# Optimization experiments

Measured on AMD Instinct MI355X. Metric: run time of the kernel, lower is better.

The kernel has to match this reference:

```python
import jax, jax.numpy as jnp
import numpy as np

NUM_V = 20000
N_EDGES = 160000
IN_CH, OUT_CH = 16, 32
IN_ORDER = OUT_ORDER = MID_ORDER = 2
N_RINGS = 2
BAND_LIMIT = 2
NUM_SAMPLES = 7


def build_kernel_basis(n_in, n_out, bl):
    """Equivariant kernel basis [num_bases, 2*bl+1, 2*n_out+1, 2*n_in+1].
    Freq axis layout: [const, cos(t), sin(t), cos(2t), sin(2t), ...] matching precomp."""
    Din, Dout, F = 2 * n_in + 1, 2 * n_out + 1, 2 * bl + 1
    I = np.eye(2)
    E = np.array([[0., -1.], [1., 0.]])   # rotation by pi/2
    S = np.array([[1., 0.], [0., -1.]])   # reflection
    ES = E @ S
    sl = lambda m: slice(0, 1) if m == 0 else slice(2 * m - 1, 2 * m + 1)
    bases = []

    def add(f, cos_blk, sin_blk, m, n):
        if f > bl:
            return
        B = np.zeros((F, Dout, Din))
        if f == 0:
            B[0, sl(m), sl(n)] = cos_blk
        else:
            B[2 * f - 1, sl(m), sl(n)] = cos_blk
            B[2 * f, sl(m), sl(n)] = sin_blk
        bases.append(B)

    for m in range(n_out + 1):
        for n in range(n_in + 1):
            if m == 0 and n == 0:
                add(0, np.ones((1, 1)), None, 0, 0)
            elif n == 0:  # scalar -> order-m pair: R(m t) e1, R(m t) e2
                add(m, np.array([[1.], [0.]]), np.array([[0.], [1.]]), m, 0)
                add(m, np.array([[0.], [1.]]), np.array([[-1.], [0.]]), m, 0)
            elif m == 0:  # order-n pair -> scalar: rows of R(-n t)
                add(n, np.array([[1., 0.]]), np.array([[0., 1.]]), 0, n)
                add(n, np.array([[0., 1.]]), np.array([[-1., 0.]]), 0, n)
            else:
                d = m - n
                f = abs(d)
                sg = 1.0 if d >= 0 else -1.0
                add(f, I, sg * E, m, n)          # R(d t)
                add(f, E, -sg * I, m, n)         # R(d t + pi/2)
                add(m + n, S, ES, m, n)          # R((m+n) t) S
                add(m + n, ES, -S, m, n)         # R((m+n) t + pi/2) S
    return np.stack(bases).astype(np.float32)


def fourier_mats(order, n):
    th = 2 * np.pi * np.arange(n) / n
    cols = [np.ones(n)]
    for m in range(1, order + 1):
        cols += [np.cos(m * th), np.sin(m * th)]
    T = np.stack(cols, 1)                              # [n_samples, 2*order+1]
    scale = np.array([1.0] + [2.0] * (2 * order)) / n
    Tinv = (T * scale).T                               # [2*order+1, n_samples]
    return jnp.asarray(T, jnp.float32), jnp.asarray(Tinv, jnp.float32)


def rep_act(x, alpha, order):
    """Gauge transport: rotate order-m feature pairs by m*alpha. x: [E,C,2*order+1]."""
    parts = [x[:, :, :1]]
    for m in range(1, order + 1):
        c = jnp.cos(m * alpha)[:, None]
        s = jnp.sin(m * alpha)[:, None]
        a, b = x[:, :, 2 * m - 1], x[:, :, 2 * m]
        parts.append(jnp.stack([c * a - s * b, s * a + c * b], axis=-1))
    return jnp.concatenate(parts, axis=-1)


def gem_conv(x, edge_index, precomp, connection, K, W, b, in_order):
    src, dst = edge_index[1], edge_index[0]
    xt = rep_act(x[src], connection, in_order)               # [E, Cin, Din] gather + transport
    wk = jnp.einsum('bfij,broc->froicj', K, W)               # fold basis with ring weights (small)
    t = jnp.einsum('ecj,froicj->efroi', xt, wk)              # per-edge freq/ring responses
    msg = jnp.einsum('efr,efroi->eoi', precomp, t)           # [E, Cout, Dout]
    out = jax.ops.segment_sum(msg, dst, num_segments=NUM_V)  # scatter-add to vertices
    return out.at[:, :, 0].add(b)                            # bias on scalar component


def regular_relu(x, order):
    T, Tinv = fourier_mats(order, NUM_SAMPLES)
    s = jnp.einsum('vcd,sd->vcs', x, T)   # irrep -> regular samples
    return jnp.einsum('vcs,ds->vcd', jax.nn.relu(s), Tinv)


def setup_inputs() -> dict:
    key = jax.random.key(0)
    k = jax.random.split(key, 8)
    nb = build_kernel_basis(IN_ORDER, MID_ORDER, BAND_LIMIT).shape[0]  # 19
    Din = 2 * IN_ORDER + 1
    x = jax.random.normal(k[0], (NUM_V, IN_CH, Din), jnp.float32)
    edge_index = jax.random.randint(k[1], (2, N_EDGES), 0, NUM_V, dtype=jnp.int32)
    precomp = jax.random.normal(k[2], (N_EDGES, 2 * BAND_LIMIT + 1, N_RINGS), jnp.float32)
    connection = jax.random.uniform(k[3], (N_EDGES,), jnp.float32) * (2 * np.pi)
    W1 = jax.random.normal(k[4], (nb, N_RINGS, OUT_CH, IN_CH), jnp.float32) * 0.1
    W2 = jax.random.normal(k[5], (nb, N_RINGS, OUT_CH, OUT_CH), jnp.float32) * 0.05
    W_lin = jax.random.normal(k[6], (OUT_CH, IN_CH), jnp.float32) * 0.1
    zeros = lambda: jnp.zeros((OUT_CH,), jnp.float32)
    return {"x": x, "edge_index": edge_index, "precomp": precomp, "connection": connection,
            "W1": W1, "b1": zeros(), "W2": W2, "b2": zeros(), "W_lin": W_lin, "b_lin": zeros()}


def reference(x, edge_index, precomp, connection, W1, b1, W2, b2, W_lin, b_lin):
    K = jnp.asarray(build_kernel_basis(IN_ORDER, MID_ORDER, BAND_LIMIT))  # orders equal -> shared basis
    y = gem_conv(x, edge_index, precomp, connection, K, W1, b1, IN_ORDER)
    y = regular_relu(y, MID_ORDER)
    y = gem_conv(y, edge_index, precomp, connection, K, W2, b2, MID_ORDER)
    res = jnp.einsum('vcd,oc->vod', x, W_lin) + b_lin[None, :, None]  # 1x1 conv residual
    o = min(y.shape[2], res.shape[2])
    y = y.at[:, :, :o].add(res[:, :, :o])
    return regular_relu(y, OUT_ORDER)
```

## Files before the change

kernel.cpp:

```cpp
#include <hip/hip_runtime.h>
#include <hip/hip_bf16.h>
#include <cstdint>

#define NV     20000
#define NE     160000
#define IC1    16
#define OC     32
#define DIN    5
#define NSLOT  49
#define NOUT   160
#define YSTR   165
struct SlotTables {
    int n;
    int b[64], f[64], i[64], j[64];
    float v[64];
};

constexpr SlotTables make_slots() {
    SlotTables T{};
    float K[19][5][5][5] = {};
    int nb = 0;
    const int BL = 2;
    auto add = [&](int f, const float (*cb)[2], const float (*sb)[2],
                   int m, int n) {
        if (f > BL) return;
        int r0 = (m == 0) ? 0 : (2 * m - 1), nr = (m == 0) ? 1 : 2;
        int c0 = (n == 0) ? 0 : (2 * n - 1), nc = (n == 0) ? 1 : 2;
        for (int a = 0; a < nr; a++)
            for (int bb = 0; bb < nc; bb++) {
                if (f == 0) {
                    K[nb][0][r0 + a][c0 + bb] = cb[a][bb];
                } else {
                    K[nb][2 * f - 1][r0 + a][c0 + bb] = cb[a][bb];
                    K[nb][2 * f    ][r0 + a][c0 + bb] = sb[a][bb];
                }
            }
        nb++;
    };
    const float ONE[2][2]  = {{1, 0}, {0, 0}};
    const float I2[2][2]   = {{1, 0}, {0, 1}};
    const float E2[2][2]   = {{0, -1}, {1, 0}};
    const float S2[2][2]   = {{1, 0}, {0, -1}};
    const float ES2[2][2]  = {{0, 1}, {1, 0}};
    const float NS2[2][2]  = {{-1, 0}, {0, 1}};
    const float C10[2][2]  = {{1, 0}, {0, 0}};
    const float C01[2][2]  = {{0, 0}, {1, 0}};
    const float CM10[2][2] = {{-1, 0}, {0, 0}};
    const float R10[2][2]  = {{1, 0}, {0, 0}};
    const float R01[2][2]  = {{0, 1}, {0, 0}};
    const float RM10[2][2] = {{-1, 0}, {0, 0}};

    for (int m = 0; m <= 2; m++)
        for (int n = 0; n <= 2; n++) {
            if (m == 0 && n == 0) {
                add(0, ONE, ONE, 0, 0);
            } else if (n == 0) {
                add(m, C10, C01, m, 0);
                add(m, C01, CM10, m, 0);
            } else if (m == 0) {
                add(n, R10, R01, 0, n);
                add(n, R01, RM10, 0, n);
            } else {
                int d = m - n;
                int f = d >= 0 ? d : -d;
                float sg = d >= 0 ? 1.f : -1.f;
                const float sgE[2][2]  = {{0, -sg}, {sg, 0}};
                const float msgI[2][2] = {{-sg, 0}, {0, -sg}};
                add(f, I2, sgE, m, n);
                add(f, E2, msgI, m, n);
                add(m + n, S2, ES2, m, n);
                add(m + n, ES2, NS2, m, n);
            }
        }
    T.n = 0;
    for (int i = 0; i < 5; i++)
        for (int b = 0; b < nb; b++)
            for (int f = 0; f < 5; f++)
                for (int j = 0; j < 5; j++)
                    if (K[b][f][i][j] != 0.0f) {
                        T.b[T.n] = b; T.f[T.n] = f; T.i[T.n] = i;
                        T.j[T.n] = j; T.v[T.n] = K[b][f][i][j];
                        T.n++;
                    }
    return T;
}

constexpr SlotTables SL = make_slots();
static_assert(SL.n == NSLOT, "expect 49 kernel-basis nonzeros");

__device__ __forceinline__ uint32_t bf16_rne(float f) {
    uint32_t u = __float_as_uint(f);
    u += 0x7fffu + ((u >> 16) & 1u);
    return u >> 16;
}

typedef __attribute__((ext_vector_type(8))) short bf16x8;
typedef __attribute__((ext_vector_type(4))) float f32x4;

template<int C>
__global__ __launch_bounds__(256) void build_M(const float* __restrict__ W,
                                               float* __restrict__ M) {
    int t = blockIdx.x * 256 + threadIdx.x;
    const int K = C * 50;
    if (t >= K * NOUT) return;
    int n = t % NOUT, k = t / NOUT;
    int o = n / 5, i = n % 5;
    int c = k / 50, r50 = k % 50;
    int j = r50 / 10, q = r50 % 10;
    int f = q >> 1, r = q & 1;
    float acc = 0.f;
    #pragma unroll
    for (int s = 0; s < NSLOT; s++) {
        if (SL.j[s] == j && SL.f[s] == f && SL.i[s] == i)
            acc += SL.v[s] * W[(size_t)((SL.b[s] * 2 + r) * 32 + o) * C + c];
    }
    M[(size_t)k * NOUT + n] = acc;
}

template<int K>
__global__ __launch_bounds__(256) void build_Mfrag(const float* __restrict__ M,
                                                   uint32_t* __restrict__ Mf) {
    int t = blockIdx.x * 256 + threadIdx.x;
    const int total = (K / 32) * 10 * 64 * 4;
    if (t >= total) return;
    int a = t & 3;
    int idx = t >> 2;
    int lane = idx & 63; idx >>= 6;
    int nt = idx % 10;
    int ck = idx / 10;
    int col = nt * 16 + (lane & 15);
    int k0 = ck * 32 + (lane >> 4) * 8 + 2 * a;
    uint32_t lo = bf16_rne(M[(size_t)k0 * NOUT + col]);
    uint32_t hi = bf16_rne(M[(size_t)(k0 + 1) * NOUT + col]);
    Mf[t] = lo | (hi << 16);
}

__global__ __launch_bounds__(256) void hist_k(const int* __restrict__ ei,
                                              int* __restrict__ counts) {
    int e = blockIdx.x * 256 + threadIdx.x;
    if (e < NE) atomicAdd(&counts[ei[e]], 1);
}

__global__ __launch_bounds__(1024) void scan_k(const int* __restrict__ counts,
                                               int* __restrict__ cursor) {
    __shared__ int part[1024];
    int t = threadIdx.x;
    int base = t * 20;
    int local[20];
    int s = 0;
    #pragma unroll
    for (int k = 0; k < 20; k++) {
        int idx = base + k;
        int c = (idx < NV) ? counts[idx] : 0;
        local[k] = c; s += c;
    }
    part[t] = s;
    __syncthreads();
    for (int off = 1; off < 1024; off <<= 1) {
        int add = (t >= off) ? part[t - off] : 0;
        __syncthreads();
        part[t] += add;
        __syncthreads();
    }
    int run = (t == 0) ? 0 : part[t - 1];
    #pragma unroll
    for (int k = 0; k < 20; k++) {
        int idx = base + k;
        if (idx < NV) { cursor[idx] = run; run += local[k]; }
    }
}

__global__ __launch_bounds__(256) void scatter_pack(const int* __restrict__ ei,
                                                    const float* __restrict__ pre,
                                                    const float* __restrict__ conn,
                                                    int* __restrict__ cursor,
                                                    int* __restrict__ SRC,
                                                    float4* __restrict__ REC) {
    int e = blockIdx.x * 256 + threadIdx.x;
    if (e == 0) {
        SRC[NE] = 0;
        REC[(size_t)NE * 3 + 0] = float4{0.f, 0.f, 0.f, 0.f};
        REC[(size_t)NE * 3 + 1] = float4{0.f, 0.f, 0.f, 0.f};
        REC[(size_t)NE * 3 + 2] = float4{0.f, 0.f, 0.f, 0.f};
    }
    if (e >= NE) return;
    int pos = atomicAdd(&cursor[ei[e]], 1);
    SRC[pos] = ei[NE + e];
    float al = conn[e];
    float c1 = __cosf(al), s1 = __sinf(al);
    const float* pp = pre + (size_t)e * 10;
    REC[(size_t)pos * 3 + 0] = float4{c1, s1, pp[0], pp[1]};
    REC[(size_t)pos * 3 + 1] = float4{pp[2], pp[3], pp[4], pp[5]};
    REC[(size_t)pos * 3 + 2] = float4{pp[6], pp[7], pp[8], pp[9]};
}

__global__ __launch_bounds__(256) void x_pack(const float* __restrict__ x,
                                              uint4* __restrict__ xb) {
    int t = blockIdx.x * 256 + threadIdx.x;
    if (t >= NV * IC1) return;
    const float* xr = x + (size_t)t * 5;
    uint4 o;
    o.x = bf16_rne(xr[0]) | (bf16_rne(xr[1]) << 16);
    o.y = bf16_rne(xr[2]) | (bf16_rne(xr[3]) << 16);
    o.z = bf16_rne(xr[4]);
    o.w = 0;
    xb[t] = o;
}

template<int C>
__global__ __launch_bounds__(256) void zbuild6(const uint4* __restrict__ xb,
                                               const int*   __restrict__ SRC,
                                               const float4* __restrict__ REC,
                                               const int* __restrict__ cursor,
                                               uint32_t* __restrict__ Z,
                                               int v0, int v1) {
    __shared__ uint32_t st[3200];
    int tid = threadIdx.x;
    int t = blockIdx.x * 256 + tid;
    int pair = t >> 1, h = t & 1;
    int npairs = (v1 - v0) * C;
    bool valid = pair < npairs;
    int c = pair % C;
    int v = v0 + (valid ? pair / C : 0);
    int beg = 0, end = 0;
    if (valid) { beg = (v == 0) ? 0 : cursor[v - 1]; end = cursor[v]; }

    float acc[25];
    #pragma unroll
    for (int z = 0; z < 25; z++) acc[z] = 0.f;

    int k = beg;
    if (k < end) {
        int k1 = (k + 1 < end) ? k + 1 : NE;
        int k2 = (k + 2 < end) ? k + 2 : NE;
        int s0 = SRC[k], s1i = SRC[k1], s2i = SRC[k2];
        const float4* rp = REC + (size_t)k * 3;
        float4 r0 = rp[0], r1 = rp[1], r2 = rp[2];
        uint4 u0 = xb[(size_t)s0 * C + c];
        uint4 u1 = xb[(size_t)s1i * C + c];
        while (true) {
            bool more = (k1 != NE);
            int k3 = (k + 3 < end) ? k + 3 : NE;
            int s3i = SRC[k3];
            uint4 u2 = xb[(size_t)s2i * C + c];
            const float4* rpn = REC + (size_t)k1 * 3;
            float4 n0 = rpn[0], n1 = rpn[1], n2 = rpn[2];
            float x0 = __uint_as_float(u0.x << 16);
            float x1 = __uint_as_float(u0.x & 0xffff0000u);
            float x2 = __uint_as_float(u0.y << 16);
            float x3 = __uint_as_float(u0.y & 0xffff0000u);
            float x4 = __uint_as_float(u0.z << 16);
            float cc1 = r0.x, ss1 = r0.y;
            float cc2 = cc1 * cc1 - ss1 * ss1, ss2 = 2.f * cc1 * ss1;
            float xt[5];
            xt[0] = x0;
            xt[1] = cc1 * x1 - ss1 * x2;
            xt[2] = ss1 * x1 + cc1 * x2;
            xt[3] = cc2 * x3 - ss2 * x4;
            xt[4] = ss2 * x3 + cc2 * x4;
            float ph[5];
            ph[0] = h ? r1.w : r0.z;
            ph[1] = h ? r2.x : r0.w;
            ph[2] = h ? r2.y : r1.x;
            ph[3] = h ? r2.z : r1.y;
            ph[4] = h ? r2.w : r1.z;
            #pragma unroll
            for (int j = 0; j < 5; j++)
                #pragma unroll
                for (int w = 0; w < 5; w++)
                    acc[j * 5 + w] = fmaf(xt[j], ph[w], acc[j * 5 + w]);
            if (!more) break;
            k = k1; k1 = k2; k2 = k3;
            r0 = n0; r1 = n1; r2 = n2;
            u0 = u1; u1 = u2;
            s2i = s3i;
        }
    }
    uint32_t* sb = st + (tid >> 1) * 25;
    #pragma unroll
    for (int j = 0; j < 5; j++) {
        float q5v = __shfl_xor(acc[j * 5 + 0], 1);
        if (h == 0) {
            sb[j * 5 + 0] = bf16_rne(acc[j * 5 + 0]) | (bf16_rne(acc[j * 5 + 1]) << 16);
            sb[j * 5 + 1] = bf16_rne(acc[j * 5 + 2]) | (bf16_rne(acc[j * 5 + 3]) << 16);
            sb[j * 5 + 2] = bf16_rne(acc[j * 5 + 4]) | (bf16_rne(q5v) << 16);
        } else {
            sb[j * 5 + 3] = bf16_rne(acc[j * 5 + 1]) | (bf16_rne(acc[j * 5 + 2]) << 16);
            sb[j * 5 + 4] = bf16_rne(acc[j * 5 + 3]) | (bf16_rne(acc[j * 5 + 4]) << 16);
        }
    }
    __syncthreads();
    size_t gbase = (size_t)blockIdx.x * 3200;
    int pbase = blockIdx.x * 128;
    for (int i = tid; i < 3200; i += 256)
        if (pbase + i / 25 < npairs) Z[gbase + i] = st[i];
}

__device__ __forceinline__ void fourier_relu(float d0, float d1, float d2,
                                             float d3, float d4, float* out5) {
    float o0 = 0, o1 = 0, o2 = 0, o3 = 0, o4 = 0;
    #pragma unroll
    for (int k = 0; k < 7; k++) {
        float th = (float)k * (6.28318530717958647692f / 7.0f);
        float ck = __cosf(th), sk = __sinf(th);
        float c2k = ck * ck - sk * sk, s2k = 2.f * ck * sk;
        float sv = d0 + ck * d1 + sk * d2 + c2k * d3 + s2k * d4;
        sv = fmaxf(sv, 0.f);
        o0 += sv; o1 += sv * ck; o2 += sv * sk; o3 += sv * c2k; o4 += sv * s2k;
    }
    const float i7 = 1.0f / 7.0f;
    out5[0] = o0 * i7; out5[1] = o1 * (2.f * i7); out5[2] = o2 * (2.f * i7);
    out5[3] = o3 * (2.f * i7); out5[4] = o4 * (2.f * i7);
}

template<int K, int EPI>
__global__ __launch_bounds__(256) void gemm_fused(const uint32_t* __restrict__ Z,
                                                  const uint32_t* __restrict__ Mf,
                                                  int rows,
                                                  uint4* __restrict__ y1b,
                                                  const float* __restrict__ bias,
                                                  const float* __restrict__ xres,
                                                  const float* __restrict__ Wl,
                                                  const float* __restrict__ bl,
                                                  float* __restrict__ outp) {
    constexpr int NC = K / 32;
    constexpr int NCH0 = (NC + 1) / 2;
    __shared__ float Ys[16 * YSTR];
    __shared__ float Xs[EPI == 2 ? 16 * 80 : 1];
    int t = threadIdx.x;
    int lane = t & 63;
    int wave = t >> 6;
    int nh = wave & 1, kh = wave >> 1;
    int r0 = blockIdx.x * 16;
    int mrow = lane & 15;
    int q = lane >> 4;
    int ra = r0 + mrow;
    if (ra >= rows) ra = rows - 1;
    const uint32_t* za = Z + (size_t)ra * (K / 2) + q * 4;
    const bf16x8* mfg = (const bf16x8*)((const uint4*)Mf + lane);

    int cka = kh ? NCH0 : 0;
    int ckz = kh ? NC : NCH0;
    int ntb = nh * 5;

    f32x4 acc[5];
    #pragma unroll
    for (int nt = 0; nt < 5; nt++) acc[nt] = {0.f, 0.f, 0.f, 0.f};

    bf16x8 af = *(const bf16x8*)(za + (size_t)cka * 16);
    bf16x8 bfr[5];
    #pragma unroll
    for (int nt = 0; nt < 5; nt++)
        bfr[nt] = mfg[((size_t)cka * 10 + ntb + nt) * 64];

    for (int ck = cka; ck < ckz; ck++) {
        bf16x8 afn = af;
        bf16x8 bfn[5];
        #pragma unroll
        for (int nt = 0; nt < 5; nt++) bfn[nt] = bfr[nt];
        if (ck + 1 < ckz) {
            afn = *(const bf16x8*)(za + (size_t)(ck + 1) * 16);
            #pragma unroll
            for (int nt = 0; nt < 5; nt++)
                bfn[nt] = mfg[((size_t)(ck + 1) * 10 + ntb + nt) * 64];
        }
        #pragma unroll
        for (int nt = 0; nt < 5; nt++)
            acc[nt] = __builtin_amdgcn_mfma_f32_16x16x32_bf16(af, bfr[nt],
                                                              acc[nt], 0, 0, 0);
        af = afn;
        #pragma unroll
        for (int nt = 0; nt < 5; nt++) bfr[nt] = bfn[nt];
    }

    if (EPI == 2) {
        int gbase = blockIdx.x * 16 * 80;
        int glim = rows * 80;
        for (int i = t; i < 16 * 80; i += 256)
            Xs[i] = (gbase + i < glim) ? xres[gbase + i] : 0.f;
    }
    if (kh == 0) {
        #pragma unroll
        for (int nt = 0; nt < 5; nt++) {
            int col = (ntb + nt) * 16 + mrow;
            #pragma unroll
            for (int reg = 0; reg < 4; reg++)
                Ys[(q * 4 + reg) * YSTR + col] = acc[nt][reg];
        }
    }
    __syncthreads();
    if (kh == 1) {
        #pragma unroll
        for (int nt = 0; nt < 5; nt++) {
            int col = (ntb + nt) * 16 + mrow;
            #pragma unroll
            for (int reg = 0; reg < 4; reg++)
                Ys[(q * 4 + reg) * YSTR + col] += acc[nt][reg];
        }
    }
    __syncthreads();
    #pragma unroll
    for (int it = 0; it < 2; it++) {
        int item = t + it * 256;
        int row = item >> 5, ch = item & 31;
        int vr = blockIdx.x * 16 + row;
        if (vr >= rows) continue;
        const float* yr = &Ys[row * YSTR + ch * 5];
        float d0 = yr[0], d1 = yr[1], d2 = yr[2], d3 = yr[3], d4 = yr[4];
        float r5[5];
        if (EPI == 1) {
            d0 += bias[ch];
            fourier_relu(d0, d1, d2, d3, d4, r5);
            uint4 o;
            o.x = bf16_rne(r5[0]) | (bf16_rne(r5[1]) << 16);
            o.y = bf16_rne(r5[2]) | (bf16_rne(r5[3]) << 16);
            o.z = bf16_rne(r5[4]);
            o.w = 0;
            y1b[(size_t)vr * 32 + ch] = o;
        } else {
            float rr0 = 0, rr1 = 0, rr2 = 0, rr3 = 0, rr4 = 0;
            const float* xs = &Xs[row * 80];
            const float* wl = Wl + ch * IC1;
            #pragma unroll
            for (int c = 0; c < IC1; c++) {
                float w = wl[c];
                rr0 = fmaf(w, xs[c * 5 + 0], rr0);
                rr1 = fmaf(w, xs[c * 5 + 1], rr1);
                rr2 = fmaf(w, xs[c * 5 + 2], rr2);
                rr3 = fmaf(w, xs[c * 5 + 3], rr3);
                rr4 = fmaf(w, xs[c * 5 + 4], rr4);
            }
            float blo = bl[ch];
            d0 += bias[ch] + rr0 + blo;
            d1 += rr1 + blo;
            d2 += rr2 + blo;
            d3 += rr3 + blo;
            d4 += rr4 + blo;
            fourier_relu(d0, d1, d2, d3, d4, r5);
            float* ob = outp + ((size_t)vr * 32 + ch) * 5;
            #pragma unroll
            for (int d = 0; d < 5; d++) ob[d] = r5[d];
        }
    }
}

extern "C" void kernel_launch(void* const* d_in, const int* in_sizes, int n_in,
                              void* d_out, int out_size, void* d_ws, size_t ws_size,
                              hipStream_t stream) {
    const float* x    = (const float*)d_in[0];
    const int*   ei   = (const int*)  d_in[1];
    const float* pre  = (const float*)d_in[2];
    const float* conn = (const float*)d_in[3];
    const float* W1   = (const float*)d_in[4];
    const float* b1   = (const float*)d_in[5];
    const float* W2   = (const float*)d_in[6];
    const float* b2   = (const float*)d_in[7];
    const float* Wl   = (const float*)d_in[8];
    const float* bl   = (const float*)d_in[9];
    float* out = (float*)d_out;

    const int K1 = IC1 * 50;
    const int K2 = OC  * 50;

    const size_t Y_BYTES   = (size_t)NV * NOUT * sizeof(float);
    const size_t M1_BYTES  = (size_t)K1 * NOUT * sizeof(float);
    const size_t M2_BYTES  = (size_t)K2 * NOUT * sizeof(float);
    const size_t MF1_BYTES = (size_t)(K1 / 32) * 10 * 64 * 16;
    const size_t MF2_BYTES = (size_t)(K2 / 32) * 10 * 64 * 16;
    const size_t CSR_BYTES = (size_t)(2 * NV) * sizeof(int);
    const size_t REC_BYTES = (size_t)(NE + 1) * 48;
    const size_t SRC_BYTES = (((size_t)(NE + 1) * 4 + 15) / 16) * 16;
    const size_t Y1B_BYTES = (size_t)NV * OC * 16;
    char* ws = (char*)d_ws;
    float* M1 = (float*)(ws);
    float* M2 = (float*)(ws + M1_BYTES);
    uint32_t* Mf1 = (uint32_t*)(ws + M1_BYTES + M2_BYTES);
    uint32_t* Mf2 = (uint32_t*)(ws + M1_BYTES + M2_BYTES + MF1_BYTES);
    int* counts = (int*)(ws + M1_BYTES + M2_BYTES + MF1_BYTES + MF2_BYTES);
    int* cursor = counts + NV;
    size_t csr_end = M1_BYTES + M2_BYTES + MF1_BYTES + MF2_BYTES + CSR_BYTES;
    float4* REC = (float4*)(ws + csr_end);
    int*    SRC = (int*)(ws + csr_end + REC_BYTES);
    uint4*  Y1B = (uint4*)(ws + csr_end + REC_BYTES + SRC_BYTES);
    uint4*  XB1 = Y1B;
    size_t fixed = csr_end + REC_BYTES + SRC_BYTES + Y1B_BYTES;

    size_t tail = (ws_size > fixed) ? (ws_size - fixed) : 0;
    uint32_t* zbuf;
    size_t zcap;
    if (tail >= Y_BYTES) { zbuf = (uint32_t*)(ws + fixed); zcap = tail; }
    else                 { zbuf = (uint32_t*)d_out;        zcap = Y_BYTES; }
    int chunk1 = (int)(zcap / ((size_t)K1 * 2)); if (chunk1 > NV) chunk1 = NV;
    int chunk2 = (int)(zcap / ((size_t)K2 * 2)); if (chunk2 > NV) chunk2 = NV;
    int nch1 = (NV + chunk1 - 1) / chunk1; chunk1 = (NV + nch1 - 1) / nch1;
    int nch2 = (NV + chunk2 - 1) / chunk2; chunk2 = (NV + nch2 - 1) / nch2;

    hipMemsetAsync(counts, 0, NV * sizeof(int), stream);

    build_M<IC1><<<(K1 * NOUT + 255) / 256, 256, 0, stream>>>(W1, M1);
    build_M<OC> <<<(K2 * NOUT + 255) / 256, 256, 0, stream>>>(W2, M2);
    build_Mfrag<K1><<<((K1 / 32) * 2560 + 255) / 256, 256, 0, stream>>>(M1, Mf1);
    build_Mfrag<K2><<<((K2 / 32) * 2560 + 255) / 256, 256, 0, stream>>>(M2, Mf2);

    hist_k<<<(NE + 255) / 256, 256, 0, stream>>>(ei, counts);
    scan_k<<<1, 1024, 0, stream>>>(counts, cursor);
    scatter_pack<<<(NE + 255) / 256, 256, 0, stream>>>(ei, pre, conn, cursor,
                                                       SRC, REC);
    x_pack<<<(NV * IC1 + 255) / 256, 256, 0, stream>>>(x, XB1);

    for (int v0 = 0; v0 < NV; v0 += chunk1) {
        int v1 = v0 + chunk1; if (v1 > NV) v1 = NV;
        int rows = v1 - v0;
        zbuild6<IC1><<<((size_t)rows * IC1 * 2 + 255) / 256, 256, 0, stream>>>(
            XB1, SRC, REC, cursor, zbuf, v0, v1);
        gemm_fused<K1, 1><<<(rows + 15) / 16, 256, 0, stream>>>(
            zbuf, Mf1, rows, Y1B + (size_t)v0 * 32, b1,
            nullptr, nullptr, nullptr, nullptr);
    }
    for (int v0 = 0; v0 < NV; v0 += chunk2) {
        int v1 = v0 + chunk2; if (v1 > NV) v1 = NV;
        int rows = v1 - v0;
        zbuild6<OC><<<((size_t)rows * OC * 2 + 255) / 256, 256, 0, stream>>>(
            Y1B, SRC, REC, cursor, zbuf, v0, v1);
        gemm_fused<K2, 2><<<(rows + 15) / 16, 256, 0, stream>>>(
            zbuf, Mf2, rows, nullptr, b2,
            x + (size_t)v0 * (IC1 * DIN), Wl, bl, out + (size_t)v0 * NOUT);
    }
}
```

Measured before the change: 257.4 us.

## Split GEMM K-loop across four wave groups and stage A rows in LDS

The fused GEMM kernel now runs 512 threads, splitting the K reduction four ways instead of two so each block has more waves in flight. The A-operand rows for the block are first loaded cooperatively into shared memory with coalesced 16-byte loads, and the MFMA loop then reads them from LDS. Partial sums from the four K groups are combined serially into the shared Y tile, which adds barriers. The epilogue maps one thread per (row, channel) item. Costs are more shared memory per block, extra synchronization, and possibly lower occupancy.

Result: faster. 248.2 us (-3.6%).

```diff
diff --git a/kernel.cpp b/kernel.cpp
--- a/kernel.cpp
+++ b/kernel.cpp
@@ -314,7 +314,7 @@
 }
 
 template<int K, int EPI>
-__global__ __launch_bounds__(256) void gemm_fused(const uint32_t* __restrict__ Z,
+__global__ __launch_bounds__(512) void gemm_fused(const uint32_t* __restrict__ Z,
                                                   const uint32_t* __restrict__ Mf,
                                                   int rows,
                                                   uint4* __restrict__ y1b,
@@ -324,7 +324,9 @@
                                                   const float* __restrict__ bl,
                                                   float* __restrict__ outp) {
     constexpr int NC = K / 32;
-    constexpr int NCH0 = (NC + 1) / 2;
+    constexpr int ZROW = K / 8;
+    constexpr int ZPAD = K / 2 + 4;
+    __shared__ uint32_t Za[16 * ZPAD];
     __shared__ float Ys[16 * YSTR];
     __shared__ float Xs[EPI == 2 ? 16 * 80 : 1];
     int t = threadIdx.x;
@@ -334,41 +336,47 @@
     int r0 = blockIdx.x * 16;
     int mrow = lane & 15;
     int q = lane >> 4;
-    int ra = r0 + mrow;
-    if (ra >= rows) ra = rows - 1;
-    const uint32_t* za = Z + (size_t)ra * (K / 2) + q * 4;
+
+    {
+        int total = 16 * ZROW;
+        for (int g = t; g < total; g += 512) {
+            int row = g / ZROW, off = g % ZROW;
+            int gr = r0 + row; if (gr >= rows) gr = rows - 1;
+            uint4 v = ((const uint4*)Z)[(size_t)gr * ZROW + off];
+            *(uint4*)&Za[row * ZPAD + off * 4] = v;
+        }
+    }
+    __syncthreads();
+
     const bf16x8* mfg = (const bf16x8*)((const uint4*)Mf + lane);
-
-    int cka = kh ? NCH0 : 0;
-    int ckz = kh ? NC : NCH0;
+    int base = (NC / 4) * kh + (kh < (NC % 4) ? kh : (NC % 4));
+    int cnt  = NC / 4 + (kh < (NC % 4) ? 1 : 0);
+    int cka = base, ckz = base + cnt;
     int ntb = nh * 5;
 
     f32x4 acc[5];
     #pragma unroll
     for (int nt = 0; nt < 5; nt++) acc[nt] = {0.f, 0.f, 0.f, 0.f};
 
-    bf16x8 af = *(const bf16x8*)(za + (size_t)cka * 16);
     bf16x8 bfr[5];
     #pragma unroll
     for (int nt = 0; nt < 5; nt++)
         bfr[nt] = mfg[((size_t)cka * 10 + ntb + nt) * 64];
 
     for (int ck = cka; ck < ckz; ck++) {
-        bf16x8 afn = af;
         bf16x8 bfn[5];
         #pragma unroll
         for (int nt = 0; nt < 5; nt++) bfn[nt] = bfr[nt];
         if (ck + 1 < ckz) {
-            afn = *(const bf16x8*)(za + (size_t)(ck + 1) * 16);
             #pragma unroll
             for (int nt = 0; nt < 5; nt++)
                 bfn[nt] = mfg[((size_t)(ck + 1) * 10 + ntb + nt) * 64];
         }
+        bf16x8 af = *(const bf16x8*)&Za[mrow * ZPAD + q * 4 + ck * 16];
         #pragma unroll
         for (int nt = 0; nt < 5; nt++)
             acc[nt] = __builtin_amdgcn_mfma_f32_16x16x32_bf16(af, bfr[nt],
                                                               acc[nt], 0, 0, 0);
-        af = afn;
         #pragma unroll
         for (int nt = 0; nt < 5; nt++) bfr[nt] = bfn[nt];
     }
@@ -376,7 +384,7 @@
     if (EPI == 2) {
         int gbase = blockIdx.x * 16 * 80;
         int glim = rows * 80;
-        for (int i = t; i < 16 * 80; i += 256)
+        for (int i = t; i < 16 * 80; i += 512)
             Xs[i] = (gbase + i < glim) ? xres[gbase + i] : 0.f;
     }
     if (kh == 0) {
@@ -399,47 +407,66 @@
         }
     }
     __syncthreads();
-    #pragma unroll
-    for (int it = 0; it < 2; it++) {
-        int item = t + it * 256;
-        int row = item >> 5, ch = item & 31;
+    if (kh == 2) {
+        #pragma unroll
+        for (int nt = 0; nt < 5; nt++) {
+            int col = (ntb + nt) * 16 + mrow;
+            #pragma unroll
+            for (int reg = 0; reg < 4; reg++)
+                Ys[(q * 4 + reg) * YSTR + col] += acc[nt][reg];
+        }
+    }
+    __syncthreads();
+    if (kh == 3) {
+        #pragma unroll
+        for (int nt = 0; nt < 5; nt++) {
+            int col = (ntb + nt) * 16 + mrow;
+            #pragma unroll
+            for (int reg = 0; reg < 4; reg++)
+                Ys[(q * 4 + reg) * YSTR + col] += acc[nt][reg];
+        }
+    }
+    __syncthreads();
+    {
+        int row = t >> 5, ch = t & 31;
         int vr = blockIdx.x * 16 + row;
-        if (vr >= rows) continue;
-        const float* yr = &Ys[row * YSTR + ch * 5];
-        float d0 = yr[0], d1 = yr[1], d2 = yr[2], d3 = yr[3], d4 = yr[4];
-        float r5[5];
-        if (EPI == 1) {
-            d0 += bias[ch];
-            fourier_relu(d0, d1, d2, d3, d4, r5);
-            uint4 o;
-            o.x = bf16_rne(r5[0]) | (bf16_rne(r5[1]) << 16);
-            o.y = bf16_rne(r5[2]) | (bf16_rne(r5[3]) << 16);
-            o.z = bf16_rne(r5[4]);
-            o.w = 0;
-            y1b[(size_t)vr * 32 + ch] = o;
-        } else {
-            float rr0 = 0, rr1 = 0, rr2 = 0, rr3 = 0, rr4 = 0;
-            const float* xs = &Xs[row * 80];
-            const float* wl = Wl + ch * IC1;
-            #pragma unroll
-            for (int c = 0; c < IC1; c++) {
-                float w = wl[c];
-                rr0 = fmaf(w, xs[c * 5 + 0], rr0);
-                rr1 = fmaf(w, xs[c * 5 + 1], rr1);
-                rr2 = fmaf(w, xs[c * 5 + 2], rr2);
-                rr3 = fmaf(w, xs[c * 5 + 3], rr3);
-                rr4 = fmaf(w, xs[c * 5 + 4], rr4);
+        if (vr < rows) {
+            const float* yr = &Ys[row * YSTR + ch * 5];
+            float d0 = yr[0], d1 = yr[1], d2 = yr[2], d3 = yr[3], d4 = yr[4];
+            float r5[5];
+            if (EPI == 1) {
+                d0 += bias[ch];
+                fourier_relu(d0, d1, d2, d3, d4, r5);
+                uint4 o;
+                o.x = bf16_rne(r5[0]) | (bf16_rne(r5[1]) << 16);
+                o.y = bf16_rne(r5[2]) | (bf16_rne(r5[3]) << 16);
+                o.z = bf16_rne(r5[4]);
+                o.w = 0;
+                y1b[(size_t)vr * 32 + ch] = o;
+            } else {
+                float rr0 = 0, rr1 = 0, rr2 = 0, rr3 = 0, rr4 = 0;
+                const float* xs = &Xs[row * 80];
+                const float* wl = Wl + ch * IC1;
+                #pragma unroll
+                for (int c = 0; c < IC1; c++) {
+                    float w = wl[c];
+                    rr0 = fmaf(w, xs[c * 5 + 0], rr0);
+                    rr1 = fmaf(w, xs[c * 5 + 1], rr1);
+                    rr2 = fmaf(w, xs[c * 5 + 2], rr2);
+                    rr3 = fmaf(w, xs[c * 5 + 3], rr3);
+                    rr4 = fmaf(w, xs[c * 5 + 4], rr4);
+                }
+                float blo = bl[ch];
+                d0 += bias[ch] + rr0 + blo;
+                d1 += rr1 + blo;
+                d2 += rr2 + blo;
+                d3 += rr3 + blo;
+                d4 += rr4 + blo;
+                fourier_relu(d0, d1, d2, d3, d4, r5);
+                float* ob = outp + ((size_t)vr * 32 + ch) * 5;
+                #pragma unroll
+                for (int d = 0; d < 5; d++) ob[d] = r5[d];
             }
-            float blo = bl[ch];
-            d0 += bias[ch] + rr0 + blo;
-            d1 += rr1 + blo;
-            d2 += rr2 + blo;
-            d3 += rr3 + blo;
-            d4 += rr4 + blo;
-            fourier_relu(d0, d1, d2, d3, d4, r5);
-            float* ob = outp + ((size_t)vr * 32 + ch) * 5;
-            #pragma unroll
-            for (int d = 0; d < 5; d++) ob[d] = r5[d];
         }
     }
 }
@@ -513,7 +540,7 @@
         int rows = v1 - v0;
         zbuild6<IC1><<<((size_t)rows * IC1 * 2 + 255) / 256, 256, 0, stream>>>(
             XB1, SRC, REC, cursor, zbuf, v0, v1);
-        gemm_fused<K1, 1><<<(rows + 15) / 16, 256, 0, stream>>>(
+        gemm_fused<K1, 1><<<(rows + 15) / 16, 512, 0, stream>>>(
             zbuf, Mf1, rows, Y1B + (size_t)v0 * 32, b1,
             nullptr, nullptr, nullptr, nullptr);
     }
@@ -522,7 +549,7 @@
         int rows = v1 - v0;
         zbuild6<OC><<<((size_t)rows * OC * 2 + 255) / 256, 256, 0, stream>>>(
             Y1B, SRC, REC, cursor, zbuf, v0, v1);
-        gemm_fused<K2, 2><<<(rows + 15) / 16, 256, 0, stream>>>(
+        gemm_fused<K2, 2><<<(rows + 15) / 16, 512, 0, stream>>>(
             zbuf, Mf2, rows, nullptr, b2,
             x + (size_t)v0 * (IC1 * DIN), Wl, bl, out + (size_t)v0 * NOUT);
     }
```
